# Optimization experiments

Hardware: AMD Instinct MI355X
Metric: run time of the kernel (lower is better)

## Reference

```python
import jax, jax.numpy as jnp
import numpy as np

ALPHA = 0.2  # LeakyReLU negative slope
N, F_IN, F_OUT = 8192, 512, 64
NEG_BIG = -9e15


def setup_inputs() -> dict:
    key = jax.random.key(0)
    k1, k2, k3, k4 = jax.random.split(key, 4)
    h = jax.random.normal(k1, (N, F_IN), dtype=jnp.float32)
    # xavier_uniform with gain 1.414
    lim_w = 1.414 * np.sqrt(6.0 / (F_IN + F_OUT))
    W = jax.random.uniform(k2, (F_IN, F_OUT), dtype=jnp.float32, minval=-lim_w, maxval=lim_w)
    lim_a = 1.414 * np.sqrt(6.0 / (2 * F_OUT + 1))
    a = jax.random.uniform(k3, (2 * F_OUT, 1), dtype=jnp.float32, minval=-lim_a, maxval=lim_a)
    adj = jax.random.randint(k4, (N, N), 0, 2, dtype=jnp.int32)
    return {"h": h, "W": W, "a": a, "adj": adj}


def reference(h, W, a, adj):
    Wh = h @ W                                  # [N, F_OUT]
    f_out = Wh.shape[1]
    a1 = a[:f_out, 0]                            # source half of attention vector
    a2 = a[f_out:, 0]                            # target half
    # e_ij = LeakyReLU(Wh_i . a1 + Wh_j . a2); equals cat([Wh_i, Wh_j]) @ a
    e = jax.nn.leaky_relu(jnp.matmul(Wh, a1)[:, None] + jnp.matmul(Wh, a2)[None, :], ALPHA)  # [N, N]
    attention = jnp.where(adj > 0, e, NEG_BIG)
    attention = jax.nn.softmax(attention, axis=1)
    # dropout is a no-op at inference (training=False)
    h_prime = attention @ Wh                     # [N, F_OUT]
    return jax.nn.elu(h_prime)                   # concat=True -> ELU
```

## Files before the change

### kernel.cpp

```cpp
#include <hip/hip_runtime.h>
#include <hip/hip_bf16.h>


typedef _Float16 f16;
typedef _Float16 f16x2 __attribute__((ext_vector_type(2)));
typedef _Float16 f16x8 __attribute__((ext_vector_type(8)));
typedef float f32x4 __attribute__((ext_vector_type(4)));

#define GAT_N 8192
#define GAT_FIN 512
#define GAT_FOUT 64
#define GAT_ALPHA 0.2f

__global__ void k0_wtrans(const float* __restrict__ W, f16* __restrict__ WT) {
    int idx = blockIdx.x * blockDim.x + threadIdx.x;
    int k = idx >> 6, c = idx & 63;
    WT[c * GAT_FIN + k] = (f16)W[idx];
}

__global__ __launch_bounds__(64) void k1_gemm(const float* __restrict__ h,
        const f16* __restrict__ WT, const float* __restrict__ a,
        f16* __restrict__ WhT, float* __restrict__ s1, float* __restrict__ s2) {
    int lane = threadIdx.x & 63;
    int l15 = lane & 15, quad = lane >> 4;
    int rb = blockIdx.x * 16;
    size_t arow = (size_t)(rb + l15) * GAT_FIN;

    f32x4 acc[4] = {};
    for (int k0 = 0; k0 < GAT_FIN; k0 += 32) {
        int kb = k0 + quad * 8;
        const float4* hp = (const float4*)(h + arow + kb);
        float4 h0 = hp[0], h1 = hp[1];
        f16x8 af = { (f16)h0.x, (f16)h0.y, (f16)h0.z, (f16)h0.w,
                     (f16)h1.x, (f16)h1.y, (f16)h1.z, (f16)h1.w };
#pragma unroll
        for (int t = 0; t < 4; t++) {
            f16x8 bf = *(const f16x8*)(WT + (t * 16 + l15) * GAT_FIN + kb);
            acc[t] = __builtin_amdgcn_mfma_f32_16x16x32_f16(af, bf, acc[t], 0, 0, 0);
        }
    }

    float a1v[4], a2v[4];
#pragma unroll
    for (int t = 0; t < 4; t++) {
        a1v[t] = a[t * 16 + l15];
        a2v[t] = a[GAT_FOUT + t * 16 + l15];
    }
#pragma unroll
    for (int reg = 0; reg < 4; reg++) {
        int r = rb + quad * 4 + reg;
        float p1 = 0.f, p2 = 0.f;
#pragma unroll
        for (int t = 0; t < 4; t++) {
            float v = acc[t][reg];
            WhT[(size_t)(t * 16 + l15) * GAT_N + r] = (f16)v;
            p1 += v * a1v[t];
            p2 += v * a2v[t];
        }
#pragma unroll
        for (int off = 1; off < 16; off <<= 1) {
            p1 += __shfl_xor(p1, off);
            p2 += __shfl_xor(p2, off);
        }
        if (l15 == 0) { s1[r] = p1; s2[r] = p2; }
    }
}

__global__ void k2_max(const float* __restrict__ s2, float* __restrict__ mx) {
    __shared__ float red[256];
    float m = -1e30f;
    for (int i = threadIdx.x; i < GAT_N; i += 256) m = fmaxf(m, s2[i]);
    red[threadIdx.x] = m;
    __syncthreads();
    for (int s = 128; s > 0; s >>= 1) {
        if (threadIdx.x < s) red[threadIdx.x] = fmaxf(red[threadIdx.x], red[threadIdx.x + s]);
        __syncthreads();
    }
    if (threadIdx.x == 0) mx[0] = red[0];
}

__global__ __launch_bounds__(512, 4) void k3_attn(const int* __restrict__ adj,
        const f16* __restrict__ WhT, const float* __restrict__ s1,
        const float* __restrict__ s2, const float* __restrict__ mxp,
        float* __restrict__ out) {
    __shared__ __align__(16) char smem[2 * 16 * 520 * 2];
    f16* pbuf = (f16*)smem;
    float (*accbuf)[16][64] = (float (*)[16][64])smem;
    __shared__ float dbuf2[16];

    int tid = threadIdx.x;
    int w = tid >> 6, lane = tid & 63;
    int l15 = lane & 15, quad = lane >> 4;
    int hhalf = lane >> 5, q = lane & 31;
    int rb = blockIdx.x * 16;
    int r = 2 * w + hhalf;

    float s1r = s1[rb + r];
    float cr = s1r + mxp[0];
    cr = fmaxf(cr, GAT_ALPHA * cr);
    const int* adjrow = adj + (size_t)(rb + r) * GAT_N;

    float dacc = 0.f;
    f32x4 acc[4] = {};
    int4   av[4];
    float4 sv[4];

    auto stage = [&](int bb) {
#pragma unroll
        for (int p = 0; p < 4; p++) {
            int   am[4]  = { av[p].x, av[p].y, av[p].z, av[p].w };
            float svv[4] = { sv[p].x, sv[p].y, sv[p].z, sv[p].w };
            int base = (4 * p + (q >> 3)) * 520 + ((q >> 1) & 3) * 128 + r * 8 + (q & 1) * 4;
            f16 pf[4];
#pragma unroll
            for (int j = 0; j < 4; j++) {
                float e = s1r + svv[j];
                e = fmaxf(e, GAT_ALPHA * e);
                float pv = __expf(e - cr);
                pv = (am[j] > 0) ? pv : 0.0f;
                dacc += pv;
                pf[j] = (f16)pv;
            }
            f16x2 lo = { pf[0], pf[1] }, hi = { pf[2], pf[3] };
            *(f16x2*)&pbuf[bb * 8320 + base]     = lo;
            *(f16x2*)&pbuf[bb * 8320 + base + 2] = hi;
        }
    };

#pragma unroll
    for (int p = 0; p < 4; p++) {
        int c0 = p * 128 + q * 4;
        av[p] = *(const int4*)(adjrow + c0);
        sv[p] = *(const float4*)(s2 + c0);
    }
    stage(0);
    __syncthreads();

    for (int rd = 0; rd < 16; rd++) {
        int b = rd & 1;
        if (rd < 15) {
#pragma unroll
            for (int p = 0; p < 4; p++) {
                int c0 = (rd + 1) * 512 + p * 128 + q * 4;
                av[p] = *(const int4*)(adjrow + c0);
                sv[p] = *(const float4*)(s2 + c0);
            }
        }
#pragma unroll
        for (int sl = 0; sl < 2; sl++) {
            int s_loc = 2 * w + sl;
            f16x8 af = *(const f16x8*)&pbuf[b * 8320 + s_loc * 520 + lane * 8];
            int kb = rd * 512 + s_loc * 32 + quad * 8;
#pragma unroll
            for (int t = 0; t < 4; t++) {
                f16x8 bf = *(const f16x8*)(WhT + (size_t)(t * 16 + l15) * GAT_N + kb);
                acc[t] = __builtin_amdgcn_mfma_f32_16x16x32_f16(af, bf, acc[t], 0, 0, 0);
            }
        }
        if (rd < 15) stage(1 - b);
        __syncthreads();
    }

#pragma unroll
    for (int t = 0; t < 4; t++)
#pragma unroll
        for (int reg = 0; reg < 4; reg++)
            accbuf[w][quad * 4 + reg][t * 16 + l15] = acc[t][reg];
#pragma unroll
    for (int off = 16; off >= 1; off >>= 1) dacc += __shfl_xor(dacc, off);
    if (q == 0) dbuf2[r] = dacc;
    __syncthreads();

    for (int o = tid; o < 16 * 64; o += 512) {
        int rr = o >> 6, c = o & 63;
        float num = 0.f;
#pragma unroll
        for (int ww = 0; ww < 8; ww++) num += accbuf[ww][rr][c];
        float hp = num / dbuf2[rr];
        out[(size_t)(rb + rr) * GAT_FOUT + c] = hp > 0.f ? hp : expm1f(hp);
    }
}

extern "C" void kernel_launch(void* const* d_in, const int* in_sizes, int n_in,
                              void* d_out, int out_size, void* d_ws, size_t ws_size,
                              hipStream_t stream) {
    const float* h   = (const float*)d_in[0];
    const float* W   = (const float*)d_in[1];
    const float* a   = (const float*)d_in[2];
    const int*   adj = (const int*)d_in[3];
    float* out = (float*)d_out;

    char* ws = (char*)d_ws;
    f16*   WT  = (f16*)ws;
    f16*   WhT = (f16*)(ws + 65536);
    float* s1  = (float*)(ws + 65536 + 1048576);
    float* s2  = (float*)(ws + 65536 + 1048576 + 32768);
    float* mx  = (float*)(ws + 65536 + 1048576 + 65536);

    k0_wtrans<<<128, 256, 0, stream>>>(W, WT);
    k1_gemm<<<512, 64, 0, stream>>>(h, WT, a, WhT, s1, s2);
    k2_max<<<1, 256, 0, stream>>>(s2, mx);
    k3_attn<<<512, 512, 0, stream>>>(adj, WhT, s1, s2, mx, out);
}
```

Baseline: 409.8 us.

## Split-K k1 GEMM across four waves, fold global max into attention kernel

The projection GEMM now uses four waves per block, each covering a quarter of K, with partial results reduced through shared memory. WhT is written as packed f16x4 and the s1/s2 dot products are reduced across waves. The single-block max kernel is removed, and every attention block recomputes the global max of s2 itself, which adds 8192 redundant reads per block but drops a serial launch. Adjacency loads become nontemporal so the streamed 256MB matrix does not pollute the cache.

```diff
diff --git a/kernel.cpp b/kernel.cpp
--- a/kernel.cpp
+++ b/kernel.cpp
@@ -4,8 +4,10 @@
 
 typedef _Float16 f16;
 typedef _Float16 f16x2 __attribute__((ext_vector_type(2)));
+typedef _Float16 f16x4 __attribute__((ext_vector_type(4)));
 typedef _Float16 f16x8 __attribute__((ext_vector_type(8)));
 typedef float f32x4 __attribute__((ext_vector_type(4)));
+typedef int   i32x4 __attribute__((ext_vector_type(4)));
 
 #define GAT_N 8192
 #define GAT_FIN 512
@@ -18,17 +20,22 @@
     WT[c * GAT_FIN + k] = (f16)W[idx];
 }
 
-__global__ __launch_bounds__(64) void k1_gemm(const float* __restrict__ h,
+__global__ __launch_bounds__(256) void k1_gemm(const float* __restrict__ h,
         const f16* __restrict__ WT, const float* __restrict__ a,
         f16* __restrict__ WhT, float* __restrict__ s1, float* __restrict__ s2) {
-    int lane = threadIdx.x & 63;
+    __shared__ float pacc[4][4][64][4];
+    __shared__ float s1red[4][16], s2red[4][16];
+
+    int tid = threadIdx.x;
+    int w = tid >> 6, lane = tid & 63;
     int l15 = lane & 15, quad = lane >> 4;
     int rb = blockIdx.x * 16;
     size_t arow = (size_t)(rb + l15) * GAT_FIN;
 
     f32x4 acc[4] = {};
-    for (int k0 = 0; k0 < GAT_FIN; k0 += 32) {
-        int kb = k0 + quad * 8;
+#pragma unroll
+    for (int ks = 0; ks < 4; ks++) {
+        int kb = w * 128 + ks * 32 + quad * 8;
         const float4* hp = (const float4*)(h + arow + kb);
         float4 h0 = hp[0], h1 = hp[1];
         f16x8 af = { (f16)h0.x, (f16)h0.y, (f16)h0.z, (f16)h0.w,
@@ -39,54 +46,52 @@
             acc[t] = __builtin_amdgcn_mfma_f32_16x16x32_f16(af, bf, acc[t], 0, 0, 0);
         }
     }
-
-    float a1v[4], a2v[4];
-#pragma unroll
-    for (int t = 0; t < 4; t++) {
-        a1v[t] = a[t * 16 + l15];
-        a2v[t] = a[GAT_FOUT + t * 16 + l15];
-    }
+#pragma unroll
+    for (int t = 0; t < 4; t++)
+        *(f32x4*)&pacc[w][t][lane][0] = acc[t];
+    __syncthreads();
+
+    float a1v = a[w * 16 + l15];
+    float a2v = a[GAT_FOUT + w * 16 + l15];
+    float vreg[4];
 #pragma unroll
     for (int reg = 0; reg < 4; reg++) {
-        int r = rb + quad * 4 + reg;
-        float p1 = 0.f, p2 = 0.f;
-#pragma unroll
-        for (int t = 0; t < 4; t++) {
-            float v = acc[t][reg];
-            WhT[(size_t)(t * 16 + l15) * GAT_N + r] = (f16)v;
-            p1 += v * a1v[t];
-            p2 += v * a2v[t];
-        }
+        float v = 0.f;
+#pragma unroll
+        for (int ww = 0; ww < 4; ww++) v += pacc[ww][w][lane][reg];
+        vreg[reg] = v;
+    }
+    f16x4 pk = { (f16)vreg[0], (f16)vreg[1], (f16)vreg[2], (f16)vreg[3] };
+    *(f16x4*)(WhT + (size_t)(w * 16 + l15) * GAT_N + rb + quad * 4) = pk;
+
+#pragma unroll
+    for (int reg = 0; reg < 4; reg++) {
+        float c1 = vreg[reg] * a1v, c2 = vreg[reg] * a2v;
 #pragma unroll
         for (int off = 1; off < 16; off <<= 1) {
-            p1 += __shfl_xor(p1, off);
-            p2 += __shfl_xor(p2, off);
-        }
-        if (l15 == 0) { s1[r] = p1; s2[r] = p2; }
-    }
-}
-
-__global__ void k2_max(const float* __restrict__ s2, float* __restrict__ mx) {
-    __shared__ float red[256];
-    float m = -1e30f;
-    for (int i = threadIdx.x; i < GAT_N; i += 256) m = fmaxf(m, s2[i]);
-    red[threadIdx.x] = m;
-    __syncthreads();
-    for (int s = 128; s > 0; s >>= 1) {
-        if (threadIdx.x < s) red[threadIdx.x] = fmaxf(red[threadIdx.x], red[threadIdx.x + s]);
-        __syncthreads();
-    }
-    if (threadIdx.x == 0) mx[0] = red[0];
+            c1 += __shfl_xor(c1, off);
+            c2 += __shfl_xor(c2, off);
+        }
+        if (l15 == 0) { s1red[w][quad * 4 + reg] = c1; s2red[w][quad * 4 + reg] = c2; }
+    }
+    __syncthreads();
+    if (tid < 16) {
+        float t1 = 0.f, t2 = 0.f;
+#pragma unroll
+        for (int ww = 0; ww < 4; ww++) { t1 += s1red[ww][tid]; t2 += s2red[ww][tid]; }
+        s1[rb + tid] = t1;
+        s2[rb + tid] = t2;
+    }
 }
 
 __global__ __launch_bounds__(512, 4) void k3_attn(const int* __restrict__ adj,
         const f16* __restrict__ WhT, const float* __restrict__ s1,
-        const float* __restrict__ s2, const float* __restrict__ mxp,
-        float* __restrict__ out) {
+        const float* __restrict__ s2, float* __restrict__ out) {
     __shared__ __align__(16) char smem[2 * 16 * 520 * 2];
     f16* pbuf = (f16*)smem;
     float (*accbuf)[16][64] = (float (*)[16][64])smem;
     __shared__ float dbuf2[16];
+    __shared__ float mred[8];
 
     int tid = threadIdx.x;
     int w = tid >> 6, lane = tid & 63;
@@ -95,20 +100,29 @@
     int rb = blockIdx.x * 16;
     int r = 2 * w + hhalf;
 
+    float m = -1e30f;
+    for (int i = tid; i < GAT_N; i += 512) m = fmaxf(m, s2[i]);
+#pragma unroll
+    for (int off = 32; off >= 1; off >>= 1) m = fmaxf(m, __shfl_xor(m, off));
+    if (lane == 0) mred[w] = m;
+    __syncthreads();
+    float mxv = mred[0];
+#pragma unroll
+    for (int ww = 1; ww < 8; ww++) mxv = fmaxf(mxv, mred[ww]);
+
     float s1r = s1[rb + r];
-    float cr = s1r + mxp[0];
+    float cr = s1r + mxv;
     cr = fmaxf(cr, GAT_ALPHA * cr);
     const int* adjrow = adj + (size_t)(rb + r) * GAT_N;
 
     float dacc = 0.f;
     f32x4 acc[4] = {};
-    int4   av[4];
+    i32x4  av[4];
     float4 sv[4];
 
     auto stage = [&](int bb) {
 #pragma unroll
         for (int p = 0; p < 4; p++) {
-            int   am[4]  = { av[p].x, av[p].y, av[p].z, av[p].w };
             float svv[4] = { sv[p].x, sv[p].y, sv[p].z, sv[p].w };
             int base = (4 * p + (q >> 3)) * 520 + ((q >> 1) & 3) * 128 + r * 8 + (q & 1) * 4;
             f16 pf[4];
@@ -117,7 +131,7 @@
                 float e = s1r + svv[j];
                 e = fmaxf(e, GAT_ALPHA * e);
                 float pv = __expf(e - cr);
-                pv = (am[j] > 0) ? pv : 0.0f;
+                pv = (av[p][j] > 0) ? pv : 0.0f;
                 dacc += pv;
                 pf[j] = (f16)pv;
             }
@@ -130,7 +144,7 @@
 #pragma unroll
     for (int p = 0; p < 4; p++) {
         int c0 = p * 128 + q * 4;
-        av[p] = *(const int4*)(adjrow + c0);
+        av[p] = __builtin_nontemporal_load((const i32x4*)(adjrow + c0));
         sv[p] = *(const float4*)(s2 + c0);
     }
     stage(0);
@@ -142,7 +156,7 @@
 #pragma unroll
             for (int p = 0; p < 4; p++) {
                 int c0 = (rd + 1) * 512 + p * 128 + q * 4;
-                av[p] = *(const int4*)(adjrow + c0);
+                av[p] = __builtin_nontemporal_load((const i32x4*)(adjrow + c0));
                 sv[p] = *(const float4*)(s2 + c0);
             }
         }
@@ -195,10 +209,8 @@
     f16*   WhT = (f16*)(ws + 65536);
     float* s1  = (float*)(ws + 65536 + 1048576);
     float* s2  = (float*)(ws + 65536 + 1048576 + 32768);
-    float* mx  = (float*)(ws + 65536 + 1048576 + 65536);
 
     k0_wtrans<<<128, 256, 0, stream>>>(W, WT);
-    k1_gemm<<<512, 64, 0, stream>>>(h, WT, a, WhT, s1, s2);
-    k2_max<<<1, 256, 0, stream>>>(s2, mx);
-    k3_attn<<<512, 512, 0, stream>>>(adj, WhT, s1, s2, mx, out);
-}
+    k1_gemm<<<512, 256, 0, stream>>>(h, WT, a, WhT, s1, s2);
+    k3_attn<<<512, 512, 0, stream>>>(adj, WhT, s1, s2, out);
+}
```

After: 407.8 us. Within noise of the previous version (-0.5%).
